# Optimization experiments

Measured on AMD Instinct MI355X. Metric: run time of the kernel, lower is better.

Reference implementation:

```python
import jax, jax.numpy as jnp
import numpy as np
from functools import partial

G, NG, H, M, MC = 8, 256, 128, 128, 64
N, S = G * NG, H
TWO_PI = 2.0 * np.pi


def setup_inputs() -> dict:
    key = jax.random.key(0)
    ks = jax.random.split(key, 10)
    node_feat = jax.random.normal(ks[0], (N, S), jnp.float32)
    positions = jax.random.uniform(ks[1], (N, 3), jnp.float32) * 10.0
    # near-orthorhombic triclinic cells, safely invertible
    cell = 10.0 * jnp.eye(3, dtype=jnp.float32)[None] + 0.5 * jax.random.normal(ks[2], (G, 3, 3), jnp.float32)
    batch = jnp.repeat(jnp.arange(G, dtype=jnp.int32), NG)
    n_vecs = jax.random.randint(ks[3], (G, M, 3), -8, 9, dtype=jnp.int32)  # integer lattice vectors
    w = jax.random.uniform(ks[4], (G, M), jnp.float32)  # Ewald k-space weights (positive)
    W_qkv = jax.random.normal(ks[5], (3 * H, H), jnp.float32) / np.sqrt(H)
    W_vg = jax.random.normal(ks[6], (H, H), jnp.float32) / np.sqrt(H)
    b_vg = jnp.full((H,), 2.0, jnp.float32)
    W_hg = jax.random.normal(ks[7], (1, H), jnp.float32) / np.sqrt(H)
    b_hg = jnp.zeros((1,), jnp.float32)
    W_mg = jax.random.normal(ks[8], (1, H), jnp.float32) / np.sqrt(H)
    b_mg = jnp.full((1,), -5.0, jnp.float32)
    return dict(node_feat=node_feat, positions=positions, cell=cell, w=w,
                W_qkv=W_qkv, W_vg=W_vg, b_vg=b_vg, W_hg=W_hg, b_hg=b_hg,
                W_mg=W_mg, b_mg=b_mg, n_vecs=n_vecs, batch=batch)


def reference(node_feat, positions, cell, w, W_qkv, W_vg, b_vg, W_hg, b_hg, W_mg, b_mg, n_vecs, batch):
    Ntot, Sdim = node_feat.shape
    Gn = cell.shape[0]
    Ng = Ntot // Gn
    Hd = Sdim  # in_proj is Identity (S == hidden)
    dtype = node_feat.dtype
    scale_q = np.float32(1.0 / np.sqrt(Hd))

    scalars = node_feat
    qkv = scalars @ W_qkv.T                      # (N, 3H)
    q, k, v = jnp.split(qkv, 3, axis=-1)
    q = jax.nn.silu(q)
    k = jax.nn.silu(k)
    v = v * jax.nn.sigmoid(scalars @ W_vg.T + b_vg)

    # per-graph blocks (batch is block-contiguous: arange(G) repeated NG times)
    qg = q.reshape(Gn, Ng, Hd)
    kg = k.reshape(Gn, Ng, Hd)
    vg = v.reshape(Gn, Ng, Hd)
    a_q, b_q = qg[..., 0::2], qg[..., 1::2]      # (G, Ng, H/2)
    a_k, b_k = kg[..., 0::2], kg[..., 1::2]

    pos_g = positions.reshape(Gn, Ng, 3)
    # fractional coords: solve(cell^T, pos^T)^T, wrapped to [0,1)
    f = jax.vmap(lambda c, p: jnp.linalg.solve(c.T, p.T).T)(cell, pos_g)
    f = f - jnp.floor(f)                         # (G, Ng, 3)

    Mtot = n_vecs.shape[1]
    n_chunks = Mtot // MC
    n_f = n_vecs.astype(dtype)
    # (n_chunks, G, MC, ...) chunk streams for scan over k-space blocks
    n_xs = n_f.reshape(Gn, n_chunks, MC, 3).swapaxes(0, 1)
    w_xs = w.reshape(Gn, n_chunks, MC).swapaxes(0, 1)
    Ng_f = jnp.asarray(Ng, dtype)

    @jax.checkpoint
    def chunk(upd, xs):
        nb, wb = xs                              # (G, MC, 3), (G, MC)
        phase = TWO_PI * jnp.einsum('gni,gmi->gmn', f, nb)   # (G, MC, Ng)
        cos = jnp.cos(phase)[..., None]          # (G, MC, Ng, 1)
        sin = jnp.sin(phase)[..., None]
        aq, bq = a_q[:, None], b_q[:, None]      # (G, 1, Ng, H/2)
        ak, bk = a_k[:, None], b_k[:, None]
        q_rot = jnp.concatenate([aq * cos - bq * sin, aq * sin + bq * cos], -1) * scale_q  # (G,MC,Ng,H)
        k_rot = jnp.concatenate([ak * cos - bk * sin, ak * sin + bk * cos], -1)
        S_blk = jnp.einsum('gmnh,gnd->gmhd', k_rot, vg) / Ng_f   # (G, MC, H, H)
        beta = jnp.einsum('gmnh,gmhd->gmnd', q_rot, S_blk)       # (G, MC, Ng, H)
        upd = upd + jnp.einsum('gm,gmnd->gnd', wb, beta)
        return upd, None

    upd0 = jnp.zeros((Gn, Ng, Hd), dtype)
    upd, _ = jax.lax.scan(chunk, upd0, (n_xs, w_xs))
    update = upd.reshape(Ntot, Hd)

    attn_gate = jnp.tanh(scalars @ W_hg.T + b_hg)      # (N, 1)
    update = update * (1.0 + 0.2 * attn_gate)
    gate_sr_lr = jax.nn.sigmoid(scalars @ W_mg.T + b_mg)
    return update, gate_sr_lr
```

## Files before the change

kernel.cpp:

```cpp
#include <hip/hip_runtime.h>
#include <math.h>

using short8 = __attribute__((ext_vector_type(8))) short;
using f32x4 = __attribute__((ext_vector_type(4))) float;

#define MFMA16(a, b, c) __builtin_amdgcn_mfma_f32_16x16x32_bf16((a), (b), (c), 0, 0, 0)

namespace {
constexpr int NG_ = 256;
constexpr int H_ = 128;
constexpr int NTOT_ = 2048;
constexpr float SCALE_E = 0.08838834764831845f / 256.0f;

constexpr size_t OFF_QA = 0;
constexpr size_t OFF_KA = 524288;
constexpr size_t OFF_VT = 1048576;
constexpr size_t OFF_CT = 1572864;
constexpr size_t OFF_ST = 2097152;
constexpr size_t OFF_E  = 2621440;
constexpr size_t OFF_GF = 3670016;
}

__device__ __forceinline__ short f2bf(float x) {
  unsigned u = __float_as_uint(x);
  unsigned r = (u + 0x7FFFu + ((u >> 16) & 1u)) >> 16;
  return (short)r;
}
__device__ __forceinline__ float bf2f(short x) {
  return __uint_as_float(((unsigned)(unsigned short)x) << 16);
}
__device__ __forceinline__ float sigmoidf_(float x) { return 1.0f / (1.0f + expf(-x)); }
__device__ __forceinline__ float siluf_(float x) { return x / (1.0f + expf(-x)); }

__device__ __forceinline__ short8 neg8(short8 x) {
  short8 r;
#pragma unroll
  for (int i = 0; i < 8; ++i) r[i] = (short)(x[i] ^ (short)0x8000);
  return r;
}
__device__ __forceinline__ short8 ldf(const short* buf, int row, int kk) {
  return *(const short8*)&buf[(row * 128 + kk) ^ ((row & 7) << 3)];
}

__global__ __launch_bounds__(512) void k_prep(
    const float* __restrict__ nf, const float* __restrict__ Wqkv,
    const float* __restrict__ Wvg, const float* __restrict__ bvg,
    const float* __restrict__ Whg, const float* __restrict__ bhg,
    const float* __restrict__ Wmg, const float* __restrict__ bmg,
    const float* __restrict__ cell, const float* __restrict__ pos,
    const int* __restrict__ nvec, const float* __restrict__ w,
    short* __restrict__ QA, short* __restrict__ KA, short* __restrict__ VT,
    short* __restrict__ CT, short* __restrict__ ST, float* __restrict__ GF,
    float* __restrict__ out_gate) {
  __shared__ short smem[49152];
  const int tid = threadIdx.x;
  const int bid = blockIdx.x;
  if (bid < 32) {
    short* lA = smem;
    short* lB = smem + 16384;
    const int r_tile = bid >> 1, h = bid & 1;
    const int n0 = r_tile * 128, c0 = h * 256;
#pragma unroll
    for (int it = 0; it < 4; ++it) {
      int e = tid + it * 512;
      int row = e >> 4, c8 = (e & 15) * 8;
      const float* src = nf + (size_t)(n0 + row) * H_ + c8;
      float4 lo = *(const float4*)src, hi = *(const float4*)(src + 4);
      short8 v;
      v[0] = f2bf(lo.x); v[1] = f2bf(lo.y); v[2] = f2bf(lo.z); v[3] = f2bf(lo.w);
      v[4] = f2bf(hi.x); v[5] = f2bf(hi.y); v[6] = f2bf(hi.z); v[7] = f2bf(hi.w);
      *(short8*)&lA[(row * 128 + c8) ^ ((row & 7) << 3)] = v;
    }
#pragma unroll
    for (int it = 0; it < 8; ++it) {
      int e = tid + it * 512;
      int row = e >> 4, c8 = (e & 15) * 8;
      int wr_g = c0 + row;
      const float* src =
          (wr_g < 384 ? Wqkv + (size_t)wr_g * H_ : Wvg + (size_t)(wr_g - 384) * H_) + c8;
      float4 lo = *(const float4*)src, hi = *(const float4*)(src + 4);
      short8 v;
      v[0] = f2bf(lo.x); v[1] = f2bf(lo.y); v[2] = f2bf(lo.z); v[3] = f2bf(lo.w);
      v[4] = f2bf(hi.x); v[5] = f2bf(hi.y); v[6] = f2bf(hi.z); v[7] = f2bf(hi.w);
      *(short8*)&lB[(row * 128 + c8) ^ ((row & 7) << 3)] = v;
    }
    __syncthreads();
    const int wid = tid >> 6, lane = tid & 63;
    const int wrow = (wid >> 2) * 64, wcol = (wid & 3) * 64;
    const int frow = lane & 15, kq = (lane >> 4) * 8;
    f32x4 acc[4][4] = {};
#pragma unroll
    for (int ks = 0; ks < 4; ++ks) {
      int kk = ks * 32 + kq;
      short8 a[4], b[4];
#pragma unroll
      for (int i = 0; i < 4; ++i) {
        a[i] = ldf(lA, wrow + i * 16 + frow, kk);
        b[i] = ldf(lB, wcol + i * 16 + frow, kk);
      }
#pragma unroll
      for (int i = 0; i < 4; ++i)
#pragma unroll
        for (int j = 0; j < 4; ++j) acc[i][j] = MFMA16(a[i], b[j], acc[i][j]);
    }
    const int orow = (lane >> 4) * 4, ocol = lane & 15;
    __syncthreads();
    if (h == 0) {
#pragma unroll
      for (int i = 0; i < 4; ++i)
#pragma unroll
        for (int j = 0; j < 4; ++j) {
          int c = wcol + j * 16 + ocol;
#pragma unroll
          for (int r = 0; r < 4; ++r) {
            int node = n0 + wrow + i * 16 + orow + r;
            float val = siluf_(acc[i][j][r]);
            if (c < 128)
              QA[(size_t)node * 128 + (c & 1) * 64 + (c >> 1)] = f2bf(val);
            else {
              int ck = c - 128;
              KA[(size_t)node * 128 + (ck & 1) * 64 + (ck >> 1)] = f2bf(val);
            }
          }
        }
    } else {
      short* gate_sh = lB;
      if (wcol >= 128) {
#pragma unroll
        for (int i = 0; i < 4; ++i)
#pragma unroll
          for (int j = 0; j < 4; ++j) {
            int d = wcol - 128 + j * 16 + ocol;
#pragma unroll
            for (int r = 0; r < 4; ++r) {
              int nl = wrow + i * 16 + orow + r;
              gate_sh[nl * 128 + d] = f2bf(sigmoidf_(acc[i][j][r] + bvg[d]));
            }
          }
      }
      __syncthreads();
      if (wcol < 128) {
        const int g_idx = n0 >> 8, half = (n0 >> 7) & 1;
#pragma unroll
        for (int i = 0; i < 4; ++i)
#pragma unroll
          for (int j = 0; j < 4; ++j) {
            int d = wcol + j * 16 + ocol;
#pragma unroll
            for (int r = 0; r < 4; ++r) {
              int nl = wrow + i * 16 + orow + r;
              float gate = bf2f(gate_sh[nl * 128 + d]);
              VT[((size_t)(g_idx * 128 + d)) * 256 + half * 128 + nl] =
                  f2bf(acc[i][j][r] * gate);
            }
          }
      }
      if (tid < 128) {
        int nl = tid;
        float hg = 0.f, mg = 0.f;
#pragma unroll 8
        for (int c = 0; c < 128; ++c) {
          float s = bf2f(lA[((nl * 128 + (c & ~7)) ^ ((nl & 7) << 3)) + (c & 7)]);
          hg += s * Whg[c];
          mg += s * Wmg[c];
        }
        int node = n0 + nl;
        GF[node] = 1.0f + 0.2f * tanhf(hg + bhg[0]);
        out_gate[node] = sigmoidf_(mg + bmg[0]);
      }
    }
  } else {
    const int b = bid - 32;
    const int g = b >> 3, n0 = (b & 7) * 32;
    float* f_sh = (float*)smem;
    int* nv_sh = (int*)((char*)smem + 512);
    float* w_sh = (float*)((char*)smem + 2048);
    if (tid < 32) {
      const float* cg = cell + (size_t)g * 9;
      float A00 = cg[0], A01 = cg[3], A02 = cg[6];
      float A10 = cg[1], A11 = cg[4], A12 = cg[7];
      float A20 = cg[2], A21 = cg[5], A22 = cg[8];
      float b00 = A11 * A22 - A12 * A21;
      float b01 = A02 * A21 - A01 * A22;
      float b02 = A01 * A12 - A02 * A11;
      float b10 = A12 * A20 - A10 * A22;
      float b11 = A00 * A22 - A02 * A20;
      float b12 = A02 * A10 - A00 * A12;
      float b20 = A10 * A21 - A11 * A20;
      float b21 = A01 * A20 - A00 * A21;
      float b22 = A00 * A11 - A01 * A10;
      float det = A00 * b00 + A01 * b10 + A02 * b20;
      float inv = 1.0f / det;
      const int node = g * NG_ + n0 + tid;
      float p0 = pos[(size_t)node * 3 + 0];
      float p1 = pos[(size_t)node * 3 + 1];
      float p2 = pos[(size_t)node * 3 + 2];
      float f0 = (b00 * p0 + b01 * p1 + b02 * p2) * inv;
      float f1 = (b10 * p0 + b11 * p1 + b12 * p2) * inv;
      float f2 = (b20 * p0 + b21 * p1 + b22 * p2) * inv;
      f_sh[tid * 4 + 0] = f0 - floorf(f0);
      f_sh[tid * 4 + 1] = f1 - floorf(f1);
      f_sh[tid * 4 + 2] = f2 - floorf(f2);
    }
    if (tid < 128) {
      nv_sh[tid * 3 + 0] = nvec[((size_t)g * 128 + tid) * 3 + 0];
      nv_sh[tid * 3 + 1] = nvec[((size_t)g * 128 + tid) * 3 + 1];
      nv_sh[tid * 3 + 2] = nvec[((size_t)g * 128 + tid) * 3 + 2];
      w_sh[tid] = sqrtf(w[(size_t)g * 128 + tid]);
    }
    __syncthreads();
    const int n_l = tid >> 4, m0 = (tid & 15) * 8;
    float f0 = f_sh[n_l * 4 + 0], f1 = f_sh[n_l * 4 + 1], f2 = f_sh[n_l * 4 + 2];
    short8 pc, ps;
#pragma unroll
    for (int i = 0; i < 8; ++i) {
      int m = m0 + i;
      float dot = f0 * (float)nv_sh[m * 3] + f1 * (float)nv_sh[m * 3 + 1] +
                  f2 * (float)nv_sh[m * 3 + 2];
      float tr = dot - floorf(dot);
      float sn = __builtin_amdgcn_sinf(tr);
      float cs = __builtin_amdgcn_cosf(tr);
      float sq = w_sh[m];
      pc[i] = f2bf(sq * cs);
      ps[i] = f2bf(sq * sn);
    }
    const int node = g * NG_ + n0 + n_l;
    *(short8*)&CT[(size_t)node * 128 + m0] = pc;
    *(short8*)&ST[(size_t)node * 128 + m0] = ps;
  }
}

__global__ __launch_bounds__(256) void k_E(
    const short* __restrict__ QA, const short* __restrict__ KA,
    const short* __restrict__ Ct, const short* __restrict__ St,
    short* __restrict__ E) {
  __shared__ short sm[49152];
  short* tQA = sm;
  short* tKA = sm + 8192;
  short* tCr = sm + 16384;
  short* tSr = sm + 24576;
  short* tCc = sm + 32768;
  short* tSc = sm + 40960;
  const int tid = threadIdx.x;
  const int R0 = blockIdx.x * 64, C0 = blockIdx.y * 64;
  const int g = blockIdx.z, gn = g * NG_;
#pragma unroll
  for (int it = 0; it < 4; ++it) {
    int e = tid + it * 256;
    int row = e >> 4, c8 = (e & 15) * 8;
    int idx = (row * 128 + c8) ^ ((row & 7) << 3);
    *(short8*)&tQA[idx] = *(const short8*)&QA[(size_t)(gn + R0 + row) * 128 + c8];
    *(short8*)&tKA[idx] = *(const short8*)&KA[(size_t)(gn + C0 + row) * 128 + c8];
    *(short8*)&tCr[idx] = *(const short8*)&Ct[(size_t)(gn + R0 + row) * 128 + c8];
    *(short8*)&tSr[idx] = *(const short8*)&St[(size_t)(gn + R0 + row) * 128 + c8];
    *(short8*)&tCc[idx] = *(const short8*)&Ct[(size_t)(gn + C0 + row) * 128 + c8];
    *(short8*)&tSc[idx] = *(const short8*)&St[(size_t)(gn + C0 + row) * 128 + c8];
  }
  __syncthreads();
  const int wid = tid >> 6, lane = tid & 63;
  const int wr = (wid >> 1) * 32, wc = (wid & 1) * 32;
  const int frow = lane & 15, kq = (lane >> 4) * 8;
  f32x4 gc[2][2] = {}, gs[2][2] = {}, cc[2][2] = {}, cs[2][2] = {};
#pragma unroll
  for (int ks = 0; ks < 4; ++ks) {
    int kk = ks * 32 + kq, kk2 = (kk + 64) & 127;
    short8 aq[2], ka[2], kb[2];
#pragma unroll
    for (int i = 0; i < 2; ++i) {
      aq[i] = ldf(tQA, wr + i * 16 + frow, kk);
      ka[i] = ldf(tKA, wc + i * 16 + frow, kk);
      short8 t = ldf(tKA, wc + i * 16 + frow, kk2);
      kb[i] = (ks >= 2) ? neg8(t) : t;
    }
#pragma unroll
    for (int i = 0; i < 2; ++i)
#pragma unroll
      for (int j = 0; j < 2; ++j) {
        gc[i][j] = MFMA16(aq[i], ka[j], gc[i][j]);
        gs[i][j] = MFMA16(aq[i], kb[j], gs[i][j]);
      }
  }
#pragma unroll
  for (int ks = 0; ks < 8; ++ks) {
    const bool lo = ks < 4;
    int kk = (ks & 3) * 32 + kq;
    short8 xr[2], yr[2], xc[2];
#pragma unroll
    for (int i = 0; i < 2; ++i) {
      short8 cr = ldf(tCr, wr + i * 16 + frow, kk);
      short8 sr = ldf(tSr, wr + i * 16 + frow, kk);
      xr[i] = lo ? cr : sr;
      yr[i] = lo ? sr : neg8(cr);
    }
#pragma unroll
    for (int j = 0; j < 2; ++j) xc[j] = ldf(lo ? tCc : tSc, wc + j * 16 + frow, kk);
#pragma unroll
    for (int i = 0; i < 2; ++i)
#pragma unroll
      for (int j = 0; j < 2; ++j) {
        cc[i][j] = MFMA16(xr[i], xc[j], cc[i][j]);
        cs[i][j] = MFMA16(yr[i], xc[j], cs[i][j]);
      }
  }
  const int orow = (lane >> 4) * 4, ocol = lane & 15;
#pragma unroll
  for (int i = 0; i < 2; ++i)
#pragma unroll
    for (int j = 0; j < 2; ++j) {
      int col = C0 + wc + j * 16 + ocol;
#pragma unroll
      for (int r = 0; r < 4; ++r) {
        int row = R0 + wr + i * 16 + orow + r;
        float e = gc[i][j][r] * cc[i][j][r] + gs[i][j][r] * cs[i][j][r];
        E[(size_t)(gn + row) * NG_ + col] = f2bf(e);
      }
    }
}

__global__ __launch_bounds__(128) void k_out(
    const short* __restrict__ E, const short* __restrict__ Vt,
    const float* __restrict__ GF, float* __restrict__ out) {
  __shared__ short lE[64 * 256];
  __shared__ short lV[64 * 256];
  const int tid = threadIdx.x;
  const int N0 = blockIdx.x * 64, D0 = blockIdx.y * 64;
  const int g = blockIdx.z;
  const int wid = tid >> 6, lane = tid & 63;
  const int wr = wid * 32;
  const int frow = lane & 15, kq = (lane >> 4) * 8;
#pragma unroll
  for (int it = 0; it < 16; ++it) {
    int e = tid + it * 128;
    int row = e >> 5, c8 = (e & 31) * 8;
    int idx = (row * 256 + c8) ^ ((row & 7) << 3);
    *(short8*)&lE[idx] = *(const short8*)&E[((size_t)g * NG_ + N0 + row) * 256 + c8];
    *(short8*)&lV[idx] = *(const short8*)&Vt[((size_t)g * 128 + D0 + row) * 256 + c8];
  }
  __syncthreads();
  f32x4 acc[2][4] = {};
#pragma unroll
  for (int ks = 0; ks < 8; ++ks) {
    int kk = ks * 32 + kq;
    short8 a[2], b[4];
#pragma unroll
    for (int i = 0; i < 2; ++i) {
      int ra = wr + i * 16 + frow;
      a[i] = *(short8*)&lE[(ra * 256 + kk) ^ ((ra & 7) << 3)];
    }
#pragma unroll
    for (int j = 0; j < 4; ++j) {
      int rb = j * 16 + frow;
      b[j] = *(short8*)&lV[(rb * 256 + kk) ^ ((rb & 7) << 3)];
    }
#pragma unroll
    for (int i = 0; i < 2; ++i)
#pragma unroll
      for (int j = 0; j < 4; ++j) acc[i][j] = MFMA16(a[i], b[j], acc[i][j]);
  }
  const int orow = (lane >> 4) * 4, ocol = lane & 15;
#pragma unroll
  for (int i = 0; i < 2; ++i)
#pragma unroll
    for (int r = 0; r < 4; ++r) {
      int gnode = g * NG_ + N0 + wr + i * 16 + orow + r;
      float fct = GF[gnode] * SCALE_E;
#pragma unroll
      for (int j = 0; j < 4; ++j) {
        out[(size_t)gnode * H_ + D0 + j * 16 + ocol] = acc[i][j][r] * fct;
      }
    }
}

extern "C" void kernel_launch(void* const* d_in, const int* in_sizes, int n_in,
                              void* d_out, int out_size, void* d_ws,
                              size_t ws_size, hipStream_t stream) {
  const float* node_feat = (const float*)d_in[0];
  const float* positions = (const float*)d_in[1];
  const float* cell = (const float*)d_in[2];
  const float* w = (const float*)d_in[3];
  const float* Wqkv = (const float*)d_in[4];
  const float* Wvg = (const float*)d_in[5];
  const float* bvg = (const float*)d_in[6];
  const float* Whg = (const float*)d_in[7];
  const float* bhg = (const float*)d_in[8];
  const float* Wmg = (const float*)d_in[9];
  const float* bmg = (const float*)d_in[10];
  const int* nvec = (const int*)d_in[11];
  float* out = (float*)d_out;
  char* ws = (char*)d_ws;

  short* QA = (short*)(ws + OFF_QA);
  short* KA = (short*)(ws + OFF_KA);
  short* VT = (short*)(ws + OFF_VT);
  short* CT = (short*)(ws + OFF_CT);
  short* ST = (short*)(ws + OFF_ST);
  short* E = (short*)(ws + OFF_E);
  float* GF = (float*)(ws + OFF_GF);

  k_prep<<<96, 512, 0, stream>>>(node_feat, Wqkv, Wvg, bvg, Whg, bhg, Wmg, bmg,
                                 cell, positions, nvec, w, QA, KA, VT, CT, ST,
                                 GF, out + (size_t)NTOT_ * H_);
  k_E<<<dim3(4, 4, 8), 256, 0, stream>>>(QA, KA, CT, ST, E);
  k_out<<<dim3(4, 2, 8), 128, 0, stream>>>(E, VT, GF, out);
}
```

Measured before the change: 28.72 us.

## Fuse prep, E and output kernels into one cooperative kernel with grid sync

Replaces the three-kernel chain with a single cooperative launch: the prep stage runs, a grid-wide sync follows, and 32 blocks then compute the E tile per 64-row slab and multiply it by V directly in shared memory, never writing E to global memory. This removes two kernel launch gaps and the E round trip through global memory. In exchange only 32 of 96 blocks do the attention phase, each looping over four column tiles serially. The grid sync also adds its own cost. The old three-kernel path is kept as a fallback if the cooperative launch fails.

```diff
diff --git a/kernel.cpp b/kernel.cpp
--- a/kernel.cpp
+++ b/kernel.cpp
@@ -1,5 +1,8 @@
 #include <hip/hip_runtime.h>
+#include <hip/hip_cooperative_groups.h>
 #include <math.h>
+
+namespace cg = cooperative_groups;
 
 using short8 = __attribute__((ext_vector_type(8))) short;
 using f32x4 = __attribute__((ext_vector_type(4))) float;
@@ -41,8 +44,12 @@
 __device__ __forceinline__ short8 ldf(const short* buf, int row, int kk) {
   return *(const short8*)&buf[(row * 128 + kk) ^ ((row & 7) << 3)];
 }
-
-__global__ __launch_bounds__(512) void k_prep(
+__device__ __forceinline__ short8 ldf64(const short* buf, int row, int kk) {
+  return *(const short8*)&buf[(row * 64 + kk) ^ ((row & 7) << 3)];
+}
+
+__device__ void prep_body(
+    int bid, int tid, short* smem,
     const float* __restrict__ nf, const float* __restrict__ Wqkv,
     const float* __restrict__ Wvg, const float* __restrict__ bvg,
     const float* __restrict__ Whg, const float* __restrict__ bhg,
@@ -52,9 +59,6 @@
     short* __restrict__ QA, short* __restrict__ KA, short* __restrict__ VT,
     short* __restrict__ CT, short* __restrict__ ST, float* __restrict__ GF,
     float* __restrict__ out_gate) {
-  __shared__ short smem[49152];
-  const int tid = threadIdx.x;
-  const int bid = blockIdx.x;
   if (bid < 32) {
     short* lA = smem;
     short* lB = smem + 16384;
@@ -230,6 +234,171 @@
   }
 }
 
+__global__ __launch_bounds__(512) void k_fused(
+    const float* __restrict__ nf, const float* __restrict__ Wqkv,
+    const float* __restrict__ Wvg, const float* __restrict__ bvg,
+    const float* __restrict__ Whg, const float* __restrict__ bhg,
+    const float* __restrict__ Wmg, const float* __restrict__ bmg,
+    const float* __restrict__ cell, const float* __restrict__ pos,
+    const int* __restrict__ nvec, const float* __restrict__ w,
+    short* __restrict__ QA, short* __restrict__ KA, short* __restrict__ VT,
+    short* __restrict__ CT, short* __restrict__ ST, float* __restrict__ GF,
+    float* __restrict__ out_gate, float* __restrict__ out) {
+  __shared__ short smem[61440];
+  const int tid = threadIdx.x;
+  const int bid = blockIdx.x;
+
+  prep_body(bid, tid, smem, nf, Wqkv, Wvg, bvg, Whg, bhg, Wmg, bmg, cell, pos,
+            nvec, w, QA, KA, VT, CT, ST, GF, out_gate);
+
+  cg::this_grid().sync();
+  if (bid >= 32) return;
+
+  short* tQA = smem;
+  short* tCr = smem + 8192;
+  short* tSr = smem + 16384;
+  short* tKA = smem + 24576;
+  short* tCc = smem + 32768;
+  short* tSc = smem + 40960;
+  short* tV  = smem + 49152;
+  short* tE  = smem + 57344;
+  const int g = bid >> 2;
+  const int R0 = (bid & 3) * 64;
+  const int gn = g * NG_;
+  const int wid = tid >> 6, lane = tid & 63;
+  const int frow = lane & 15, kq = (lane >> 4) * 8;
+  const int orow = (lane >> 4) * 4, ocol = lane & 15;
+  const int pr = (wid >> 2) * 32, pd = (wid & 3) * 32;
+  const int wr2 = (wid >> 1) * 32, wc2 = (wid & 1) * 32;
+
+#pragma unroll
+  for (int it = 0; it < 2; ++it) {
+    int e = tid + it * 512;
+    int row = e >> 4, c8 = (e & 15) * 8;
+    int idx = (row * 128 + c8) ^ ((row & 7) << 3);
+    size_t ga = (size_t)(gn + R0 + row) * 128 + c8;
+    *(short8*)&tQA[idx] = *(const short8*)&QA[ga];
+    *(short8*)&tCr[idx] = *(const short8*)&CT[ga];
+    *(short8*)&tSr[idx] = *(const short8*)&ST[ga];
+  }
+
+  f32x4 oacc[2][2] = {};
+  for (int c4 = 0; c4 < 4; ++c4) {
+    const int C0 = c4 * 64;
+    __syncthreads();
+#pragma unroll
+    for (int it = 0; it < 2; ++it) {
+      int e = tid + it * 512;
+      int row = e >> 4, c8 = (e & 15) * 8;
+      int idx = (row * 128 + c8) ^ ((row & 7) << 3);
+      size_t ga = (size_t)(gn + C0 + row) * 128 + c8;
+      *(short8*)&tKA[idx] = *(const short8*)&KA[ga];
+      *(short8*)&tCc[idx] = *(const short8*)&CT[ga];
+      *(short8*)&tSc[idx] = *(const short8*)&ST[ga];
+      int d = e >> 3, n8 = (e & 7) * 8;
+      *(short8*)&tV[(d * 64 + n8) ^ ((d & 7) << 3)] =
+          *(const short8*)&VT[((size_t)g * 128 + d) * 256 + C0 + n8];
+    }
+    __syncthreads();
+    if (wid < 4) {
+      f32x4 gc[2][2] = {}, gs[2][2] = {}, qc[2][2] = {}, qs[2][2] = {};
+#pragma unroll
+      for (int ks = 0; ks < 4; ++ks) {
+        int kk = ks * 32 + kq, kk2 = (kk + 64) & 127;
+        short8 aq[2], ka[2], kb[2];
+#pragma unroll
+        for (int i = 0; i < 2; ++i) {
+          aq[i] = ldf(tQA, wr2 + i * 16 + frow, kk);
+          ka[i] = ldf(tKA, wc2 + i * 16 + frow, kk);
+          short8 t = ldf(tKA, wc2 + i * 16 + frow, kk2);
+          kb[i] = (ks >= 2) ? neg8(t) : t;
+        }
+#pragma unroll
+        for (int i = 0; i < 2; ++i)
+#pragma unroll
+          for (int j = 0; j < 2; ++j) {
+            gc[i][j] = MFMA16(aq[i], ka[j], gc[i][j]);
+            gs[i][j] = MFMA16(aq[i], kb[j], gs[i][j]);
+          }
+      }
+#pragma unroll
+      for (int ks = 0; ks < 8; ++ks) {
+        const bool lo = ks < 4;
+        int kk = (ks & 3) * 32 + kq;
+        short8 xr[2], yr[2], xc[2];
+#pragma unroll
+        for (int i = 0; i < 2; ++i) {
+          short8 cr = ldf(tCr, wr2 + i * 16 + frow, kk);
+          short8 sr = ldf(tSr, wr2 + i * 16 + frow, kk);
+          xr[i] = lo ? cr : sr;
+          yr[i] = lo ? sr : neg8(cr);
+        }
+#pragma unroll
+        for (int j = 0; j < 2; ++j)
+          xc[j] = ldf(lo ? tCc : tSc, wc2 + j * 16 + frow, kk);
+#pragma unroll
+        for (int i = 0; i < 2; ++i)
+#pragma unroll
+          for (int j = 0; j < 2; ++j) {
+            qc[i][j] = MFMA16(xr[i], xc[j], qc[i][j]);
+            qs[i][j] = MFMA16(yr[i], xc[j], qs[i][j]);
+          }
+      }
+#pragma unroll
+      for (int i = 0; i < 2; ++i)
+#pragma unroll
+        for (int j = 0; j < 2; ++j) {
+          int col = wc2 + j * 16 + ocol;
+#pragma unroll
+          for (int r = 0; r < 4; ++r) {
+            int row = wr2 + i * 16 + orow + r;
+            float ev = gc[i][j][r] * qc[i][j][r] + gs[i][j][r] * qs[i][j][r];
+            tE[(row * 64 + col) ^ ((row & 7) << 3)] = f2bf(ev);
+          }
+        }
+    }
+    __syncthreads();
+#pragma unroll
+    for (int ks = 0; ks < 2; ++ks) {
+      int kk = ks * 32 + kq;
+      short8 a[2], b[2];
+#pragma unroll
+      for (int i = 0; i < 2; ++i) a[i] = ldf64(tE, pr + i * 16 + frow, kk);
+#pragma unroll
+      for (int j = 0; j < 2; ++j) b[j] = ldf64(tV, pd + j * 16 + frow, kk);
+#pragma unroll
+      for (int i = 0; i < 2; ++i)
+#pragma unroll
+        for (int j = 0; j < 2; ++j) oacc[i][j] = MFMA16(a[i], b[j], oacc[i][j]);
+    }
+  }
+#pragma unroll
+  for (int i = 0; i < 2; ++i)
+#pragma unroll
+    for (int r = 0; r < 4; ++r) {
+      int node = gn + R0 + pr + i * 16 + orow + r;
+      float fct = GF[node] * SCALE_E;
+#pragma unroll
+      for (int j = 0; j < 2; ++j)
+        out[(size_t)node * H_ + pd + j * 16 + ocol] = oacc[i][j][r] * fct;
+    }
+}
+
+__global__ __launch_bounds__(512) void k_prep(
+    const float* __restrict__ nf, const float* __restrict__ Wqkv,
+    const float* __restrict__ Wvg, const float* __restrict__ bvg,
+    const float* __restrict__ Whg, const float* __restrict__ bhg,
+    const float* __restrict__ Wmg, const float* __restrict__ bmg,
+    const float* __restrict__ cell, const float* __restrict__ pos,
+    const int* __restrict__ nvec, const float* __restrict__ w,
+    short* __restrict__ QA, short* __restrict__ KA, short* __restrict__ VT,
+    short* __restrict__ CT, short* __restrict__ ST, float* __restrict__ GF,
+    float* __restrict__ out_gate) {
+  __shared__ short smem[49152];
+  prep_body(blockIdx.x, threadIdx.x, smem, nf, Wqkv, Wvg, bvg, Whg, bhg, Wmg,
+            bmg, cell, pos, nvec, w, QA, KA, VT, CT, ST, GF, out_gate);
+}
+
 __global__ __launch_bounds__(256) void k_E(
     const short* __restrict__ QA, const short* __restrict__ KA,
     const short* __restrict__ Ct, const short* __restrict__ St,
@@ -396,10 +565,20 @@
   short* ST = (short*)(ws + OFF_ST);
   short* E = (short*)(ws + OFF_E);
   float* GF = (float*)(ws + OFF_GF);
-
-  k_prep<<<96, 512, 0, stream>>>(node_feat, Wqkv, Wvg, bvg, Whg, bhg, Wmg, bmg,
-                                 cell, positions, nvec, w, QA, KA, VT, CT, ST,
-                                 GF, out + (size_t)NTOT_ * H_);
-  k_E<<<dim3(4, 4, 8), 256, 0, stream>>>(QA, KA, CT, ST, E);
-  k_out<<<dim3(4, 2, 8), 128, 0, stream>>>(E, VT, GF, out);
-}
+  float* out_gate = out + (size_t)NTOT_ * H_;
+
+  void* kp[] = {(void*)&node_feat, (void*)&Wqkv, (void*)&Wvg, (void*)&bvg,
+                (void*)&Whg,       (void*)&bhg,  (void*)&Wmg, (void*)&bmg,
+                (void*)&cell,      (void*)&positions, (void*)&nvec, (void*)&w,
+                (void*)&QA,        (void*)&KA,   (void*)&VT,  (void*)&CT,
+                (void*)&ST,        (void*)&GF,   (void*)&out_gate, (void*)&out};
+  hipError_t err = hipLaunchCooperativeKernel((const void*)k_fused, dim3(96),
+                                              dim3(512), kp, 0, stream);
+  if (err != hipSuccess) {
+    k_prep<<<96, 512, 0, stream>>>(node_feat, Wqkv, Wvg, bvg, Whg, bhg, Wmg,
+                                   bmg, cell, positions, nvec, w, QA, KA, VT,
+                                   CT, ST, GF, out_gate);
+    k_E<<<dim3(4, 4, 8), 256, 0, stream>>>(QA, KA, CT, ST, E);
+    k_out<<<dim3(4, 2, 8), 128, 0, stream>>>(E, VT, GF, out);
+  }
+}
```

Result: slower. 66.74 us (+132.4%).

## Fuse E-matrix and value-projection kernels into one flash-style kernel

Applied to the files above, without the earlier changes.

Merges the kernel that builds the per-graph attention-like matrix E with the kernel that multiplies E by V. Each block now owns 32 query rows of one graph and loops over 64-column chunks, keeping E in shared memory and accumulating the output in registers. This removes the global round trip of E and one kernel launch. In exchange the grid drops to 64 blocks with a serial four-step loop and extra barriers, which lowers parallelism.

```diff
diff --git a/kernel.cpp b/kernel.cpp
--- a/kernel.cpp
+++ b/kernel.cpp
@@ -17,8 +17,7 @@
 constexpr size_t OFF_VT = 1048576;
 constexpr size_t OFF_CT = 1572864;
 constexpr size_t OFF_ST = 2097152;
-constexpr size_t OFF_E  = 2621440;
-constexpr size_t OFF_GF = 3670016;
+constexpr size_t OFF_GF = 2621440;
 }
 
 __device__ __forceinline__ short f2bf(float x) {
@@ -40,6 +39,9 @@
 }
 __device__ __forceinline__ short8 ldf(const short* buf, int row, int kk) {
   return *(const short8*)&buf[(row * 128 + kk) ^ ((row & 7) << 3)];
+}
+__device__ __forceinline__ short8 ldf64(const short* buf, int row, int kk) {
+  return *(const short8*)&buf[(row * 64 + kk) ^ ((row & 7) << 3)];
 }
 
 __global__ __launch_bounds__(512) void k_prep(
@@ -230,145 +232,110 @@
   }
 }
 
-__global__ __launch_bounds__(256) void k_E(
+__global__ __launch_bounds__(512) void k_EV(
     const short* __restrict__ QA, const short* __restrict__ KA,
-    const short* __restrict__ Ct, const short* __restrict__ St,
-    short* __restrict__ E) {
-  __shared__ short sm[49152];
-  short* tQA = sm;
-  short* tKA = sm + 8192;
-  short* tCr = sm + 16384;
-  short* tSr = sm + 24576;
-  short* tCc = sm + 32768;
-  short* tSc = sm + 40960;
+    const short* __restrict__ VT, const short* __restrict__ CT,
+    const short* __restrict__ ST, const float* __restrict__ GF,
+    float* __restrict__ out) {
+  __shared__ short smem[47104];
+  short* tQ  = smem;
+  short* tCr = smem + 4096;
+  short* tSr = smem + 8192;
+  short* tKA = smem + 12288;
+  short* tCc = smem + 20480;
+  short* tSc = smem + 28672;
+  short* tV  = smem + 36864;
+  short* tE  = smem + 45056;
   const int tid = threadIdx.x;
-  const int R0 = blockIdx.x * 64, C0 = blockIdx.y * 64;
-  const int g = blockIdx.z, gn = g * NG_;
-#pragma unroll
-  for (int it = 0; it < 4; ++it) {
-    int e = tid + it * 256;
-    int row = e >> 4, c8 = (e & 15) * 8;
+  const int bid = blockIdx.x;
+  const int g = bid >> 3;
+  const int R0 = (bid & 7) * 32;
+  const int gn = g * NG_;
+  const int wid = tid >> 6, lane = tid & 63;
+  const int frow = lane & 15, kq = (lane >> 4) * 8;
+  const int orow = (lane >> 4) * 4, ocol = lane & 15;
+  const int rfrag = wid >> 2;
+  const int cfrag = wid & 3;
+
+  {
+    int row = tid >> 4, c8 = (tid & 15) * 8;
     int idx = (row * 128 + c8) ^ ((row & 7) << 3);
-    *(short8*)&tQA[idx] = *(const short8*)&QA[(size_t)(gn + R0 + row) * 128 + c8];
-    *(short8*)&tKA[idx] = *(const short8*)&KA[(size_t)(gn + C0 + row) * 128 + c8];
-    *(short8*)&tCr[idx] = *(const short8*)&Ct[(size_t)(gn + R0 + row) * 128 + c8];
-    *(short8*)&tSr[idx] = *(const short8*)&St[(size_t)(gn + R0 + row) * 128 + c8];
-    *(short8*)&tCc[idx] = *(const short8*)&Ct[(size_t)(gn + C0 + row) * 128 + c8];
-    *(short8*)&tSc[idx] = *(const short8*)&St[(size_t)(gn + C0 + row) * 128 + c8];
+    size_t ga = (size_t)(gn + R0 + row) * 128 + c8;
+    *(short8*)&tQ[idx] = *(const short8*)&QA[ga];
+    *(short8*)&tCr[idx] = *(const short8*)&CT[ga];
+    *(short8*)&tSr[idx] = *(const short8*)&ST[ga];
   }
-  __syncthreads();
-  const int wid = tid >> 6, lane = tid & 63;
-  const int wr = (wid >> 1) * 32, wc = (wid & 1) * 32;
-  const int frow = lane & 15, kq = (lane >> 4) * 8;
-  f32x4 gc[2][2] = {}, gs[2][2] = {}, cc[2][2] = {}, cs[2][2] = {};
-#pragma unroll
-  for (int ks = 0; ks < 4; ++ks) {
-    int kk = ks * 32 + kq, kk2 = (kk + 64) & 127;
-    short8 aq[2], ka[2], kb[2];
-#pragma unroll
-    for (int i = 0; i < 2; ++i) {
-      aq[i] = ldf(tQA, wr + i * 16 + frow, kk);
-      ka[i] = ldf(tKA, wc + i * 16 + frow, kk);
-      short8 t = ldf(tKA, wc + i * 16 + frow, kk2);
-      kb[i] = (ks >= 2) ? neg8(t) : t;
-    }
-#pragma unroll
-    for (int i = 0; i < 2; ++i)
+
+  f32x4 oacc[2] = {};
+  for (int c4 = 0; c4 < 4; ++c4) {
+    const int C0 = c4 * 64;
+    __syncthreads();
+#pragma unroll
+    for (int it = 0; it < 2; ++it) {
+      int e = tid + it * 512;
+      int row = e >> 4, c8 = (e & 15) * 8;
+      int idx = (row * 128 + c8) ^ ((row & 7) << 3);
+      size_t ga = (size_t)(gn + C0 + row) * 128 + c8;
+      *(short8*)&tKA[idx] = *(const short8*)&KA[ga];
+      *(short8*)&tCc[idx] = *(const short8*)&CT[ga];
+      *(short8*)&tSc[idx] = *(const short8*)&ST[ga];
+      int d = e >> 3, n8 = (e & 7) * 8;
+      *(short8*)&tV[(d * 64 + n8) ^ ((d & 7) << 3)] =
+          *(const short8*)&VT[((size_t)g * 128 + d) * 256 + C0 + n8];
+    }
+    __syncthreads();
+    f32x4 gc = {}, gs = {}, qc = {}, qs = {};
+#pragma unroll
+    for (int ks = 0; ks < 4; ++ks) {
+      int kk = ks * 32 + kq, kk2 = (kk + 64) & 127;
+      short8 aq = ldf(tQ, rfrag * 16 + frow, kk);
+      short8 ka = ldf(tKA, cfrag * 16 + frow, kk);
+      short8 t = ldf(tKA, cfrag * 16 + frow, kk2);
+      short8 kb = (ks >= 2) ? neg8(t) : t;
+      gc = MFMA16(aq, ka, gc);
+      gs = MFMA16(aq, kb, gs);
+    }
+#pragma unroll
+    for (int ks = 0; ks < 8; ++ks) {
+      const bool lo = ks < 4;
+      int kk = (ks & 3) * 32 + kq;
+      short8 cr = ldf(tCr, rfrag * 16 + frow, kk);
+      short8 sr = ldf(tSr, rfrag * 16 + frow, kk);
+      short8 xr = lo ? cr : sr;
+      short8 yr = lo ? sr : neg8(cr);
+      short8 xc = ldf(lo ? tCc : tSc, cfrag * 16 + frow, kk);
+      qc = MFMA16(xr, xc, qc);
+      qs = MFMA16(yr, xc, qs);
+    }
+    {
+      int col = cfrag * 16 + ocol;
+#pragma unroll
+      for (int r = 0; r < 4; ++r) {
+        int row = rfrag * 16 + orow + r;
+        float ev = gc[r] * qc[r] + gs[r] * qs[r];
+        tE[(row * 64 + col) ^ ((row & 7) << 3)] = f2bf(ev);
+      }
+    }
+    __syncthreads();
+#pragma unroll
+    for (int ks = 0; ks < 2; ++ks) {
+      int kk = ks * 32 + kq;
+      short8 a = ldf64(tE, rfrag * 16 + frow, kk);
 #pragma unroll
       for (int j = 0; j < 2; ++j) {
-        gc[i][j] = MFMA16(aq[i], ka[j], gc[i][j]);
-        gs[i][j] = MFMA16(aq[i], kb[j], gs[i][j]);
-      }
+        short8 b = ldf64(tV, cfrag * 32 + j * 16 + frow, kk);
+        oacc[j] = MFMA16(a, b, oacc[j]);
+      }
+    }
   }
 #pragma unroll
-  for (int ks = 0; ks < 8; ++ks) {
-    const bool lo = ks < 4;
-    int kk = (ks & 3) * 32 + kq;
-    short8 xr[2], yr[2], xc[2];
-#pragma unroll
-    for (int i = 0; i < 2; ++i) {
-      short8 cr = ldf(tCr, wr + i * 16 + frow, kk);
-      short8 sr = ldf(tSr, wr + i * 16 + frow, kk);
-      xr[i] = lo ? cr : sr;
-      yr[i] = lo ? sr : neg8(cr);
-    }
-#pragma unroll
-    for (int j = 0; j < 2; ++j) xc[j] = ldf(lo ? tCc : tSc, wc + j * 16 + frow, kk);
-#pragma unroll
-    for (int i = 0; i < 2; ++i)
-#pragma unroll
-      for (int j = 0; j < 2; ++j) {
-        cc[i][j] = MFMA16(xr[i], xc[j], cc[i][j]);
-        cs[i][j] = MFMA16(yr[i], xc[j], cs[i][j]);
-      }
+  for (int r = 0; r < 4; ++r) {
+    int node = gn + R0 + rfrag * 16 + orow + r;
+    float fct = GF[node] * SCALE_E;
+#pragma unroll
+    for (int j = 0; j < 2; ++j)
+      out[(size_t)node * H_ + cfrag * 32 + j * 16 + ocol] = oacc[j][r] * fct;
   }
-  const int orow = (lane >> 4) * 4, ocol = lane & 15;
-#pragma unroll
-  for (int i = 0; i < 2; ++i)
-#pragma unroll
-    for (int j = 0; j < 2; ++j) {
-      int col = C0 + wc + j * 16 + ocol;
-#pragma unroll
-      for (int r = 0; r < 4; ++r) {
-        int row = R0 + wr + i * 16 + orow + r;
-        float e = gc[i][j][r] * cc[i][j][r] + gs[i][j][r] * cs[i][j][r];
-        E[(size_t)(gn + row) * NG_ + col] = f2bf(e);
-      }
-    }
-}
-
-__global__ __launch_bounds__(128) void k_out(
-    const short* __restrict__ E, const short* __restrict__ Vt,
-    const float* __restrict__ GF, float* __restrict__ out) {
-  __shared__ short lE[64 * 256];
-  __shared__ short lV[64 * 256];
-  const int tid = threadIdx.x;
-  const int N0 = blockIdx.x * 64, D0 = blockIdx.y * 64;
-  const int g = blockIdx.z;
-  const int wid = tid >> 6, lane = tid & 63;
-  const int wr = wid * 32;
-  const int frow = lane & 15, kq = (lane >> 4) * 8;
-#pragma unroll
-  for (int it = 0; it < 16; ++it) {
-    int e = tid + it * 128;
-    int row = e >> 5, c8 = (e & 31) * 8;
-    int idx = (row * 256 + c8) ^ ((row & 7) << 3);
-    *(short8*)&lE[idx] = *(const short8*)&E[((size_t)g * NG_ + N0 + row) * 256 + c8];
-    *(short8*)&lV[idx] = *(const short8*)&Vt[((size_t)g * 128 + D0 + row) * 256 + c8];
-  }
-  __syncthreads();
-  f32x4 acc[2][4] = {};
-#pragma unroll
-  for (int ks = 0; ks < 8; ++ks) {
-    int kk = ks * 32 + kq;
-    short8 a[2], b[4];
-#pragma unroll
-    for (int i = 0; i < 2; ++i) {
-      int ra = wr + i * 16 + frow;
-      a[i] = *(short8*)&lE[(ra * 256 + kk) ^ ((ra & 7) << 3)];
-    }
-#pragma unroll
-    for (int j = 0; j < 4; ++j) {
-      int rb = j * 16 + frow;
-      b[j] = *(short8*)&lV[(rb * 256 + kk) ^ ((rb & 7) << 3)];
-    }
-#pragma unroll
-    for (int i = 0; i < 2; ++i)
-#pragma unroll
-      for (int j = 0; j < 4; ++j) acc[i][j] = MFMA16(a[i], b[j], acc[i][j]);
-  }
-  const int orow = (lane >> 4) * 4, ocol = lane & 15;
-#pragma unroll
-  for (int i = 0; i < 2; ++i)
-#pragma unroll
-    for (int r = 0; r < 4; ++r) {
-      int gnode = g * NG_ + N0 + wr + i * 16 + orow + r;
-      float fct = GF[gnode] * SCALE_E;
-#pragma unroll
-      for (int j = 0; j < 4; ++j) {
-        out[(size_t)gnode * H_ + D0 + j * 16 + ocol] = acc[i][j][r] * fct;
-      }
-    }
 }
 
 extern "C" void kernel_launch(void* const* d_in, const int* in_sizes, int n_in,
@@ -394,12 +361,11 @@
   short* VT = (short*)(ws + OFF_VT);
   short* CT = (short*)(ws + OFF_CT);
   short* ST = (short*)(ws + OFF_ST);
-  short* E = (short*)(ws + OFF_E);
   float* GF = (float*)(ws + OFF_GF);
+  float* out_gate = out + (size_t)NTOT_ * H_;
 
   k_prep<<<96, 512, 0, stream>>>(node_feat, Wqkv, Wvg, bvg, Whg, bhg, Wmg, bmg,
                                  cell, positions, nvec, w, QA, KA, VT, CT, ST,
-                                 GF, out + (size_t)NTOT_ * H_);
-  k_E<<<dim3(4, 4, 8), 256, 0, stream>>>(QA, KA, CT, ST, E);
-  k_out<<<dim3(4, 2, 8), 128, 0, stream>>>(E, VT, GF, out);
-}
+                                 GF, out_gate);
+  k_EV<<<64, 512, 0, stream>>>(QA, KA, VT, CT, ST, GF, out);
+}
```

After: 31.23 us. +8.8%, slower.
